# Optimization experiments

Measured on AMD Instinct MI355X. Metric: run time of the kernel, lower is better.

The kernel has to match this reference:

```python
import jax, jax.numpy as jnp
import numpy as np

SCALE_FACTOR = 4.0
DROPOUT_P = 0.5
DROPOUT_KEY = jax.random.key(42)  # fixed key: torch dropout is stochastic; we fix RNG for reproducibility


def setup_inputs() -> dict:
    key = jax.random.key(0)
    k1, k2 = jax.random.split(key)
    x1 = jax.random.normal(k1, (4096, 1024), dtype=jnp.float32)
    x2 = jax.random.normal(k2, (4096, 1024), dtype=jnp.float32)
    return {"x1": x1, "x2": x2}


def reference(x1, x2):
    # scores: [M, N] = x1 @ x2^T, scaled
    scores = jnp.matmul(x1, x2.T) * SCALE_FACTOR
    # F.softmax with no dim on 2-D input -> softmax over dim 1 (keys)
    attn = jax.nn.softmax(scores, axis=-1)
    # dropout p=0.5, train mode (inverted dropout: scale kept units by 1/(1-p))
    keep = jax.random.bernoulli(DROPOUT_KEY, 1.0 - DROPOUT_P, attn.shape)
    attn = jnp.where(keep, attn / (1.0 - DROPOUT_P), 0.0).astype(attn.dtype)
    # output: [M, D] = attn @ x2 (x2 reused as values)
    return jnp.matmul(attn, x2)
```

## Files before the change

### kernel.cpp

```cpp
#include <hip/hip_runtime.h>

typedef unsigned short u16;
typedef unsigned int   u32;
typedef __attribute__((ext_vector_type(4))) float f32x4;
typedef __attribute__((ext_vector_type(8))) short bf16x8;
typedef __attribute__((ext_vector_type(8))) unsigned short u16x8;
typedef __attribute__((ext_vector_type(4))) unsigned short u16x4;

#define MROWS 4096
#define DDIM  1024

__device__ __forceinline__ u16 f2bf(float f) {
  u32 u = __float_as_uint(f);
  return (u16)((u + 0x7FFFu + ((u >> 16) & 1u)) >> 16);
}
__device__ __forceinline__ float bf2f(u16 h) { return __uint_as_float(((u32)h) << 16); }

__device__ __forceinline__ u32 rotl32(u32 x, int r) { return (x << r) | (x >> (32 - r)); }
__device__ __forceinline__ u32 threefry_bits(u32 n) {
  const u32 K0 = 0u, K1 = 42u, K2 = 0x1BD11BDAu ^ 0u ^ 42u;
  u32 x0 = K0;
  u32 x1 = n + K1;
#define TF4(a,b,c,d) \
  x0 += x1; x1 = rotl32(x1, a); x1 ^= x0; \
  x0 += x1; x1 = rotl32(x1, b); x1 ^= x0; \
  x0 += x1; x1 = rotl32(x1, c); x1 ^= x0; \
  x0 += x1; x1 = rotl32(x1, d); x1 ^= x0;
  TF4(13,15,26,6);  x0 += K1; x1 += K2 + 1u;
  TF4(17,29,16,24); x0 += K2; x1 += K0 + 2u;
  TF4(13,15,26,6);  x0 += K0; x1 += K1 + 3u;
  TF4(17,29,16,24); x0 += K1; x1 += K2 + 4u;
  TF4(13,15,26,6);  x0 += K2; x1 += K0 + 5u;
#undef TF4
  return x0 ^ x1;
}

__global__ __launch_bounds__(256)
void expandA(const float4* __restrict__ x, u16* __restrict__ out) {
  int t = blockIdx.x * 256 + threadIdx.x;
  float4 v0 = x[(size_t)t * 2], v1 = x[(size_t)t * 2 + 1];
  float vv[8] = {v0.x*4.f, v0.y*4.f, v0.z*4.f, v0.w*4.f,
                 v1.x*4.f, v1.y*4.f, v1.z*4.f, v1.w*4.f};
  u16 o[24];
#pragma unroll
  for (int j = 0; j < 8; ++j) {
    u16 h = f2bf(vv[j]);
    u16 l = f2bf(vv[j] - bf2f(h));
    o[3*j] = h; o[3*j+1] = h; o[3*j+2] = l;
  }
  u16x8* dst = (u16x8*)(out + (size_t)t * 24);
#pragma unroll
  for (int q = 0; q < 3; ++q) {
    u16x8 wv;
#pragma unroll
    for (int j = 0; j < 8; ++j) wv[j] = o[q*8+j];
    dst[q] = wv;
  }
}

__global__ __launch_bounds__(256)
void castB_transpose(const float* __restrict__ x2, u16* __restrict__ XB,
                     u16* __restrict__ VT) {
  __shared__ float tile[64][65];
  int tid = threadIdx.x;
  int dt = blockIdx.x;
  int kt = blockIdx.y;
#pragma unroll
  for (int it = 0; it < 16; ++it) {
    int lin = it * 256 + tid;
    int r = lin >> 6, c = lin & 63;
    tile[r][c] = x2[(size_t)(kt*64 + r) * DDIM + dt*64 + c];
  }
  __syncthreads();
#pragma unroll
  for (int itr = 0; itr < 2; ++itr) {
    int r  = (tid >> 3) + itr * 32;
    int c0 = (tid & 7) * 8;
    u16 o[24];
#pragma unroll
    for (int j = 0; j < 8; ++j) {
      float v = tile[r][c0 + j];
      u16 h = f2bf(v);
      u16 l = f2bf(v - bf2f(h));
      o[3*j] = h; o[3*j+1] = l; o[3*j+2] = h;
    }
    u16x8* dst = (u16x8*)(XB + (size_t)(kt*64 + r) * 3072 + (size_t)(dt*64 + c0) * 3);
#pragma unroll
    for (int q = 0; q < 3; ++q) {
      u16x8 wv;
#pragma unroll
      for (int j = 0; j < 8; ++j) wv[j] = o[q*8+j];
      dst[q] = wv;
    }
  }
#pragma unroll
  for (int it = 0; it < 2; ++it) {
    int dr  = (tid >> 3) + it * 32;
    int kc0 = (tid & 7) * 8;
    u16x8 wv;
#pragma unroll
    for (int j = 0; j < 8; ++j) wv[j] = f2bf(tile[kc0 + j][dr]);
    *(u16x8*)(VT + (size_t)(dt*64 + dr) * MROWS + kt*64 + kc0) = wv;
  }
}

__device__ __forceinline__ void gload16(const u16* g, u16* l) {
  __builtin_amdgcn_global_load_lds(
      (const __attribute__((address_space(1))) void*)g,
      (__attribute__((address_space(3))) void*)l, 16, 0, 0);
}

#define BARRIER() do { asm volatile("" ::: "memory"); __builtin_amdgcn_s_barrier(); \
                       asm volatile("" ::: "memory"); } while (0)
#define VMCNT(N)  asm volatile("s_waitcnt vmcnt(" #N ")" ::: "memory")
#define PRIO1()   __builtin_amdgcn_s_setprio(1)
#define PRIO0()   __builtin_amdgcn_s_setprio(0)

__device__ __forceinline__ void mma_quad(f32x4 (&acc)[8][4], const bf16x8 (&aF)[4][2],
                                         const bf16x8 (&bF)[2][2], int MH, int NH) {
#pragma unroll
  for (int kx = 0; kx < 2; ++kx)
#pragma unroll
    for (int m = 0; m < 4; ++m)
#pragma unroll
      for (int n = 0; n < 2; ++n)
        acc[MH*4+m][NH*2+n] = __builtin_amdgcn_mfma_f32_16x16x32_bf16(
            aF[m][kx], bF[n][kx], acc[MH*4+m][NH*2+n], 0, 0, 0);
}

template <bool OUT16, bool REMAP>
__device__ __forceinline__ void gemm_body(const u16* __restrict__ A,
                                          const u16* __restrict__ Bt,
                                          void* __restrict__ Cv,
                                          int M, int N, int K, int ntpc) {
  __shared__ u16 smem[65536];
  const int tid = threadIdx.x;
  const int lane = tid & 63;
  const int w = tid >> 6;
  const int wr = w >> 2;
  const int wc = w & 3;
  const int fr = lane & 15;
  const int hi = lane >> 4;

  int bxi, byi;
  if (REMAP) {
    const int id0 = blockIdx.y * gridDim.x + blockIdx.x;
    const int c = id0 & 7, j = id0 >> 3;
    bxi = j >> 1;
    byi = c * 2 + (j & 1);
  } else {
    bxi = blockIdx.x; byi = blockIdx.y;
  }

  const long bm = (long)byi * 256;
  const long bn = (long)bxi * 256;
  const size_t kcol0 = (size_t)blockIdx.z * ntpc * 64;

  const int srow = tid >> 3;
  const int scol = (((tid & 7) ^ (srow & 7)) << 3);
  const u16* Abase = A  + (size_t)(bm + srow) * K + kcol0 + scol;
  const u16* Bbase = Bt + (size_t)(bn + srow) * K + kcol0 + scol;

  const int csw0 = ((hi)     ^ (fr & 7)) << 3;
  const int csw1 = ((4 + hi) ^ (fr & 7)) << 3;
  const int arow = (wr*16 + fr) * 64;
  const int brow = (wc*16 + fr) * 64;

#define RD_A2(dst, D, H, M0) do { \
    const u16* _p = smem + ((D)*2+(H))*8192 + arow + (M0)*2048; \
    dst[M0][0]   = *(const bf16x8*)(_p + csw0); \
    dst[M0][1]   = *(const bf16x8*)(_p + csw1); \
    dst[M0+1][0] = *(const bf16x8*)(_p + 2048 + csw0); \
    dst[M0+1][1] = *(const bf16x8*)(_p + 2048 + csw1); } while (0)
#define RD_B(dst, D, H) do { \
    const u16* _p = smem + 32768 + ((D)*2+(H))*8192 + brow; \
    dst[0][0] = *(const bf16x8*)(_p + csw0); \
    dst[0][1] = *(const bf16x8*)(_p + csw1); \
    dst[1][0] = *(const bf16x8*)(_p + 4096 + csw0); \
    dst[1][1] = *(const bf16x8*)(_p + 4096 + csw1); } while (0)

  f32x4 acc[8][4];
#pragma unroll
  for (int m = 0; m < 8; ++m)
#pragma unroll
    for (int n = 0; n < 4; ++n) acc[m][n] = (f32x4){0.f, 0.f, 0.f, 0.f};
  bf16x8 a0[4][2], a1[4][2], b0[2][2], b1[2][2];

#define STAGE_A(TAU,H,D) do { \
    const u16* _s = Abase + (size_t)(H)*128*K + (size_t)(TAU)*64; \
    u16* _d = smem + ((D)*2+(H))*8192 + tid*8; \
    gload16(_s, _d); gload16(_s + (size_t)64*K, _d + 4096); } while (0)
#define STAGE_B(TAU,H,D) do { \
    const u16* _s = Bbase + (size_t)(H)*128*K + (size_t)(TAU)*64; \
    u16* _d = smem + 32768 + ((D)*2+(H))*8192 + tid*8; \
    gload16(_s, _d); gload16(_s + (size_t)64*K, _d + 4096); } while (0)

  STAGE_A(0,0,0); STAGE_B(0,0,0);
  STAGE_B(0,1,0); STAGE_A(0,1,0);
  VMCNT(0); BARRIER();
  RD_A2(a0,0,0,0); RD_A2(a0,0,0,2); RD_B(b0,0,0);
  STAGE_A(1,0,1); STAGE_B(1,0,1);
  STAGE_B(1,1,1);
  STAGE_A(1,1,1);
  BARRIER();

  const int nt = ntpc;
  for (int T = 0; T < nt; T += 2) {
    const int t2 = (T + 2 < nt) ? T + 2 : nt - 1;
    const int t3 = (T + 3 < nt) ? T + 3 : nt - 1;

    RD_B(b1, 0, 1); RD_A2(a1, 0, 1, 0);
    PRIO1(); mma_quad(acc, a0, b0, 0, 0); PRIO0();
    BARRIER();
    RD_A2(a1, 0, 1, 2);
    STAGE_A(t2, 0, 0); STAGE_B(t2, 0, 0);
    PRIO1(); mma_quad(acc, a0, b1, 0, 1); PRIO0();
    VMCNT(10); BARRIER();
    RD_A2(a0, 1, 0, 0);
    STAGE_B(t2, 1, 0);
    PRIO1(); mma_quad(acc, a1, b0, 1, 0); PRIO0();
    VMCNT(10); BARRIER();
    RD_A2(a0, 1, 0, 2); RD_B(b0, 1, 0);
    STAGE_A(t2, 1, 0);
    PRIO1(); mma_quad(acc, a1, b1, 1, 1); PRIO0();
    VMCNT(8); BARRIER();
    RD_B(b1, 1, 1); RD_A2(a1, 1, 1, 0);
    PRIO1(); mma_quad(acc, a0, b0, 0, 0); PRIO0();
    BARRIER();
    RD_A2(a1, 1, 1, 2);
    STAGE_A(t3, 0, 1); STAGE_B(t3, 0, 1);
    PRIO1(); mma_quad(acc, a0, b1, 0, 1); PRIO0();
    VMCNT(10); BARRIER();
    RD_A2(a0, 0, 0, 0);
    STAGE_B(t3, 1, 1);
    PRIO1(); mma_quad(acc, a1, b0, 1, 0); PRIO0();
    VMCNT(10); BARRIER();
    RD_A2(a0, 0, 0, 2); RD_B(b0, 0, 0);
    STAGE_A(t3, 1, 1);
    PRIO1(); mma_quad(acc, a1, b1, 1, 1); PRIO0();
    VMCNT(8); BARRIER();
  }
#undef STAGE_A
#undef STAGE_B
#undef RD_A2
#undef RD_B

#pragma unroll
  for (int m = 0; m < 8; ++m)
#pragma unroll
    for (int n = 0; n < 4; ++n) {
      size_t row0 = (size_t)(bm + m*32 + wr*16 + hi*4);
      size_t col  = (size_t)(bn + n*64 + wc*16 + fr);
#pragma unroll
      for (int r = 0; r < 4; ++r) {
        if (OUT16) {
          u16* Cz = (u16*)Cv + (size_t)blockIdx.z * (size_t)M * N;
          Cz[(row0 + r) * N + col] = f2bf(acc[m][n][r]);
        } else {
          float* Cz = (float*)Cv + (size_t)blockIdx.z * (size_t)M * N;
          Cz[(row0 + r) * N + col] = acc[m][n][r];
        }
      }
    }
}

__global__ __launch_bounds__(512, 2)
void gemm_qk(const u16* __restrict__ A, const u16* __restrict__ Bt,
             void* __restrict__ Cv, int M, int N, int K, int ntpc) {
  gemm_body<false, false>(A, Bt, Cv, M, N, K, ntpc);
}
__global__ __launch_bounds__(512, 2)
void gemm_pv(const u16* __restrict__ A, const u16* __restrict__ Bt,
             void* __restrict__ Cv, int M, int N, int K, int ntpc) {
  gemm_body<true, true>(A, Bt, Cv, M, N, K, ntpc);
}

__global__ __launch_bounds__(256)
void softmax_dropout(const float* __restrict__ S, u16* __restrict__ P) {
  const int tid  = threadIdx.x;
  const int lane = tid & 63;
  const int w    = tid >> 6;
  const int row  = blockIdx.x * 4 + w;
  const float4* Sr = (const float4*)(S + (size_t)row * MROWS);
  float4 v[16];
#pragma unroll
  for (int i = 0; i < 16; ++i) v[i] = Sr[i * 64 + lane];
  float m = -3.0e38f;
#pragma unroll
  for (int i = 0; i < 16; ++i)
    m = fmaxf(m, fmaxf(fmaxf(v[i].x, v[i].y), fmaxf(v[i].z, v[i].w)));
#pragma unroll
  for (int off = 32; off > 0; off >>= 1) m = fmaxf(m, __shfl_xor(m, off, 64));
  float s = 0.0f;
#pragma unroll
  for (int i = 0; i < 16; ++i) {
    v[i].x = __expf(v[i].x - m); v[i].y = __expf(v[i].y - m);
    v[i].z = __expf(v[i].z - m); v[i].w = __expf(v[i].w - m);
    s += v[i].x + v[i].y + v[i].z + v[i].w;
  }
#pragma unroll
  for (int off = 32; off > 0; off >>= 1) s += __shfl_xor(s, off, 64);
  const float inv = 2.0f / s;
  u16* Pr = P + (size_t)row * MROWS;
#pragma unroll
  for (int i = 0; i < 16; ++i) {
    int j0 = (i * 64 + lane) * 4;
    u32 base = (u32)row * 4096u + (u32)j0;
    float e[4] = {v[i].x, v[i].y, v[i].z, v[i].w};
    u16x4 o;
#pragma unroll
    for (int c = 0; c < 4; ++c) {
      u32 bits = threefry_bits(base + (u32)c);
      float val = (bits & 0x80000000u) ? 0.0f : e[c] * inv;
      o[c] = f2bf(val);
    }
    *(u16x4*)(Pr + j0) = o;
  }
}

__global__ __launch_bounds__(256)
void reduce4(const u16* __restrict__ p, float4* __restrict__ out) {
  size_t i = (size_t)blockIdx.x * 256 + threadIdx.x;
  const size_t NP = (size_t)MROWS * DDIM;
  u16x4 a = *(const u16x4*)(p + i*4);
  u16x4 b = *(const u16x4*)(p + NP + i*4);
  u16x4 c = *(const u16x4*)(p + 2*NP + i*4);
  u16x4 d = *(const u16x4*)(p + 3*NP + i*4);
  float4 r;
  r.x = bf2f(a[0]) + bf2f(b[0]) + bf2f(c[0]) + bf2f(d[0]);
  r.y = bf2f(a[1]) + bf2f(b[1]) + bf2f(c[1]) + bf2f(d[1]);
  r.z = bf2f(a[2]) + bf2f(b[2]) + bf2f(c[2]) + bf2f(d[2]);
  r.w = bf2f(a[3]) + bf2f(b[3]) + bf2f(c[3]) + bf2f(d[3]);
  out[i] = r;
}

extern "C" void kernel_launch(void* const* d_in, const int* in_sizes, int n_in,
                              void* d_out, int out_size, void* d_ws, size_t ws_size,
                              hipStream_t stream) {
  const float* x1 = (const float*)d_in[0];
  const float* x2 = (const float*)d_in[1];
  float* out = (float*)d_out;
  char* ws = (char*)d_ws;

  const size_t OFF_XB   = 25165824;
  const size_t OFF_VT   = 50331648;
  const size_t OFF_S    = 58720256;
  const size_t NEED     = 125829120;
  if (ws_size < NEED) {
    hipMemsetAsync(d_out, 0x7F, (size_t)out_size * sizeof(float), stream);
    return;
  }
  u16*   XA = (u16*)(ws);
  u16*   XB = (u16*)(ws + OFF_XB);
  u16*   VT = (u16*)(ws + OFF_VT);
  float* S  = (float*)(ws + OFF_S);
  u16*   PT = (u16*)(ws + OFF_S);
  u16*   P  = (u16*)(ws);

  expandA<<<2048, 256, 0, stream>>>((const float4*)x1, XA);
  castB_transpose<<<dim3(16, 64), 256, 0, stream>>>(x2, XB, VT);
  gemm_qk<<<dim3(16, 16, 1), 512, 0, stream>>>(XA, XB, S, 4096, 4096, 3072, 48);
  softmax_dropout<<<1024, 256, 0, stream>>>(S, P);
  gemm_pv<<<dim3(4, 16, 4), 512, 0, stream>>>(P, VT, PT, 4096, 1024, 4096, 16);
  reduce4<<<4096, 256, 0, stream>>>(PT, (float4*)out);
}
```

Before: 186.4 us.

## Restructure GEMM to 256x128 tiles, 4 waves, triple-buffered BK=32 pipeline

Replaces the 256x256, 8-wave, double-buffered BK=64 GEMM with a 256x128 tile computed by 4 waves (each 128x64), using a three-stage LDS ring of BK=32 slices and a simpler two-phase loop. Both GEMMs now launch twice as many blocks, and a generalized XCD-aware block remap replaces the old one. The aim is a smaller LDS footprint, more blocks for occupancy, and a simpler prefetch schedule. In exchange each block reuses fewer bytes per tile and runs more K iterations.

```diff
diff --git a/kernel.cpp b/kernel.cpp
--- a/kernel.cpp
+++ b/kernel.cpp
@@ -116,141 +116,107 @@
 #define PRIO1()   __builtin_amdgcn_s_setprio(1)
 #define PRIO0()   __builtin_amdgcn_s_setprio(0)
 
-__device__ __forceinline__ void mma_quad(f32x4 (&acc)[8][4], const bf16x8 (&aF)[4][2],
-                                         const bf16x8 (&bF)[2][2], int MH, int NH) {
-#pragma unroll
-  for (int kx = 0; kx < 2; ++kx)
-#pragma unroll
-    for (int m = 0; m < 4; ++m)
-#pragma unroll
-      for (int n = 0; n < 2; ++n)
-        acc[MH*4+m][NH*2+n] = __builtin_amdgcn_mfma_f32_16x16x32_bf16(
-            aF[m][kx], bF[n][kx], acc[MH*4+m][NH*2+n], 0, 0, 0);
-}
-
-template <bool OUT16, bool REMAP>
+template <bool OUT16>
 __device__ __forceinline__ void gemm_body(const u16* __restrict__ A,
                                           const u16* __restrict__ Bt,
                                           void* __restrict__ Cv,
-                                          int M, int N, int K, int ntpc) {
-  __shared__ u16 smem[65536];
-  const int tid = threadIdx.x;
+                                          int M, int N, int K, int ntpc, int gxlog) {
+  __shared__ u16 smem[36864];
+  const int tid  = threadIdx.x;
   const int lane = tid & 63;
-  const int w = tid >> 6;
-  const int wr = w >> 2;
-  const int wc = w & 3;
+  const int w    = tid >> 6;
+  const int wm = w >> 1;
+  const int wn = w & 1;
   const int fr = lane & 15;
   const int hi = lane >> 4;
 
-  int bxi, byi;
-  if (REMAP) {
-    const int id0 = blockIdx.y * gridDim.x + blockIdx.x;
-    const int c = id0 & 7, j = id0 >> 3;
-    bxi = j >> 1;
-    byi = c * 2 + (j & 1);
-  } else {
-    bxi = blockIdx.x; byi = blockIdx.y;
-  }
+  const int id0 = blockIdx.y * gridDim.x + blockIdx.x;
+  const int xcd = id0 & 7, j = id0 >> 3;
+  const int bxi = j & (gridDim.x - 1);
+  const int byi = xcd * (gridDim.y >> 3) + (j >> gxlog);
 
   const long bm = (long)byi * 256;
-  const long bn = (long)bxi * 256;
-  const size_t kcol0 = (size_t)blockIdx.z * ntpc * 64;
-
-  const int srow = tid >> 3;
-  const int scol = (((tid & 7) ^ (srow & 7)) << 3);
-  const u16* Abase = A  + (size_t)(bm + srow) * K + kcol0 + scol;
-  const u16* Bbase = Bt + (size_t)(bn + srow) * K + kcol0 + scol;
-
-  const int csw0 = ((hi)     ^ (fr & 7)) << 3;
-  const int csw1 = ((4 + hi) ^ (fr & 7)) << 3;
-  const int arow = (wr*16 + fr) * 64;
-  const int brow = (wc*16 + fr) * 64;
-
-#define RD_A2(dst, D, H, M0) do { \
-    const u16* _p = smem + ((D)*2+(H))*8192 + arow + (M0)*2048; \
-    dst[M0][0]   = *(const bf16x8*)(_p + csw0); \
-    dst[M0][1]   = *(const bf16x8*)(_p + csw1); \
-    dst[M0+1][0] = *(const bf16x8*)(_p + 2048 + csw0); \
-    dst[M0+1][1] = *(const bf16x8*)(_p + 2048 + csw1); } while (0)
-#define RD_B(dst, D, H) do { \
-    const u16* _p = smem + 32768 + ((D)*2+(H))*8192 + brow; \
-    dst[0][0] = *(const bf16x8*)(_p + csw0); \
-    dst[0][1] = *(const bf16x8*)(_p + csw1); \
-    dst[1][0] = *(const bf16x8*)(_p + 4096 + csw0); \
-    dst[1][1] = *(const bf16x8*)(_p + 4096 + csw1); } while (0)
+  const long bn = (long)bxi * 128;
+  const size_t kcol0 = (size_t)blockIdx.z * ntpc * 32;
+
+  const int srow = lane >> 2;
+  const int schunk = (lane & 3) ^ (srow & 3);
+  const u16* asrc = A  + (size_t)(bm + w*64 + srow) * K + kcol0 + schunk*8;
+  const u16* bsrc = Bt + (size_t)(bn + w*32 + srow) * K + kcol0 + schunk*8;
+
+  const int csw  = (hi ^ (fr & 3)) << 3;
+  const int aoff = (wm*128 + fr) * 32 + csw;
+  const int boff = 8192 + (wn*64 + fr) * 32 + csw;
+  const int adst = w*2048 + lane*8;
+  const int bdst = 8192 + w*1024 + lane*8;
 
   f32x4 acc[8][4];
 #pragma unroll
   for (int m = 0; m < 8; ++m)
 #pragma unroll
     for (int n = 0; n < 4; ++n) acc[m][n] = (f32x4){0.f, 0.f, 0.f, 0.f};
-  bf16x8 a0[4][2], a1[4][2], b0[2][2], b1[2][2];
-
-#define STAGE_A(TAU,H,D) do { \
-    const u16* _s = Abase + (size_t)(H)*128*K + (size_t)(TAU)*64; \
-    u16* _d = smem + ((D)*2+(H))*8192 + tid*8; \
-    gload16(_s, _d); gload16(_s + (size_t)64*K, _d + 4096); } while (0)
-#define STAGE_B(TAU,H,D) do { \
-    const u16* _s = Bbase + (size_t)(H)*128*K + (size_t)(TAU)*64; \
-    u16* _d = smem + 32768 + ((D)*2+(H))*8192 + tid*8; \
-    gload16(_s, _d); gload16(_s + (size_t)64*K, _d + 4096); } while (0)
-
-  STAGE_A(0,0,0); STAGE_B(0,0,0);
-  STAGE_B(0,1,0); STAGE_A(0,1,0);
-  VMCNT(0); BARRIER();
-  RD_A2(a0,0,0,0); RD_A2(a0,0,0,2); RD_B(b0,0,0);
-  STAGE_A(1,0,1); STAGE_B(1,0,1);
-  STAGE_B(1,1,1);
-  STAGE_A(1,1,1);
-  BARRIER();
+  bf16x8 a0[8], a1[8], b0[4], b1[4];
+
+#define STAGE(TAU, LB) do { \
+    const u16* _a = asrc + (size_t)(TAU)*32; \
+    const u16* _b = bsrc + (size_t)(TAU)*32; \
+    gload16(_a,                 smem + (LB) + adst); \
+    gload16(_a + (size_t)16*K,  smem + (LB) + adst + 512); \
+    gload16(_a + (size_t)32*K,  smem + (LB) + adst + 1024); \
+    gload16(_a + (size_t)48*K,  smem + (LB) + adst + 1536); \
+    gload16(_b,                 smem + (LB) + bdst); \
+    gload16(_b + (size_t)16*K,  smem + (LB) + bdst + 512); } while (0)
+
+#define RD(dA, dB, LB) do { \
+    const u16* _pa = smem + (LB) + aoff; \
+    const u16* _pb = smem + (LB) + boff; \
+    dA[0] = *(const bf16x8*)(_pa);        dA[1] = *(const bf16x8*)(_pa + 512); \
+    dA[2] = *(const bf16x8*)(_pa + 1024); dA[3] = *(const bf16x8*)(_pa + 1536); \
+    dA[4] = *(const bf16x8*)(_pa + 2048); dA[5] = *(const bf16x8*)(_pa + 2560); \
+    dA[6] = *(const bf16x8*)(_pa + 3072); dA[7] = *(const bf16x8*)(_pa + 3584); \
+    dB[0] = *(const bf16x8*)(_pb);        dB[1] = *(const bf16x8*)(_pb + 512); \
+    dB[2] = *(const bf16x8*)(_pb + 1024); dB[3] = *(const bf16x8*)(_pb + 1536); } while (0)
+
+#define MMA(aa, bb) do { PRIO1(); \
+    _Pragma("unroll") \
+    for (int m = 0; m < 8; ++m) \
+      _Pragma("unroll") \
+      for (int n = 0; n < 4; ++n) \
+        acc[m][n] = __builtin_amdgcn_mfma_f32_16x16x32_bf16(aa[m], bb[n], acc[m][n], 0, 0, 0); \
+    PRIO0(); } while (0)
+
+  u32 lb0 = 0, lb1 = 12288, lb2 = 24576;
+
+  STAGE(0, lb0); STAGE(1, lb1); STAGE(2, lb2);
+  VMCNT(12); BARRIER();
+  RD(a0, b0, lb0);
+  VMCNT(6); BARRIER();
 
   const int nt = ntpc;
   for (int T = 0; T < nt; T += 2) {
-    const int t2 = (T + 2 < nt) ? T + 2 : nt - 1;
     const int t3 = (T + 3 < nt) ? T + 3 : nt - 1;
-
-    RD_B(b1, 0, 1); RD_A2(a1, 0, 1, 0);
-    PRIO1(); mma_quad(acc, a0, b0, 0, 0); PRIO0();
-    BARRIER();
-    RD_A2(a1, 0, 1, 2);
-    STAGE_A(t2, 0, 0); STAGE_B(t2, 0, 0);
-    PRIO1(); mma_quad(acc, a0, b1, 0, 1); PRIO0();
-    VMCNT(10); BARRIER();
-    RD_A2(a0, 1, 0, 0);
-    STAGE_B(t2, 1, 0);
-    PRIO1(); mma_quad(acc, a1, b0, 1, 0); PRIO0();
-    VMCNT(10); BARRIER();
-    RD_A2(a0, 1, 0, 2); RD_B(b0, 1, 0);
-    STAGE_A(t2, 1, 0);
-    PRIO1(); mma_quad(acc, a1, b1, 1, 1); PRIO0();
-    VMCNT(8); BARRIER();
-    RD_B(b1, 1, 1); RD_A2(a1, 1, 1, 0);
-    PRIO1(); mma_quad(acc, a0, b0, 0, 0); PRIO0();
-    BARRIER();
-    RD_A2(a1, 1, 1, 2);
-    STAGE_A(t3, 0, 1); STAGE_B(t3, 0, 1);
-    PRIO1(); mma_quad(acc, a0, b1, 0, 1); PRIO0();
-    VMCNT(10); BARRIER();
-    RD_A2(a0, 0, 0, 0);
-    STAGE_B(t3, 1, 1);
-    PRIO1(); mma_quad(acc, a1, b0, 1, 0); PRIO0();
-    VMCNT(10); BARRIER();
-    RD_A2(a0, 0, 0, 2); RD_B(b0, 0, 0);
-    STAGE_A(t3, 1, 1);
-    PRIO1(); mma_quad(acc, a1, b1, 1, 1); PRIO0();
-    VMCNT(8); BARRIER();
-  }
-#undef STAGE_A
-#undef STAGE_B
-#undef RD_A2
-#undef RD_B
+    const int t4 = (T + 4 < nt) ? T + 4 : nt - 1;
+
+    RD(a1, b1, lb1);
+    STAGE(t3, lb0);
+    MMA(a0, b0);
+    VMCNT(6); BARRIER();
+    RD(a0, b0, lb2);
+    STAGE(t4, lb1);
+    MMA(a1, b1);
+    VMCNT(6); BARRIER();
+    u32 tmp = lb2; lb2 = lb1; lb1 = lb0; lb0 = tmp;
+  }
+#undef STAGE
+#undef RD
+#undef MMA
 
 #pragma unroll
   for (int m = 0; m < 8; ++m)
 #pragma unroll
     for (int n = 0; n < 4; ++n) {
-      size_t row0 = (size_t)(bm + m*32 + wr*16 + hi*4);
-      size_t col  = (size_t)(bn + n*64 + wc*16 + fr);
+      size_t row0 = (size_t)(bm + wm*128 + m*16 + hi*4);
+      size_t col  = (size_t)(bn + wn*64 + n*16 + fr);
 #pragma unroll
       for (int r = 0; r < 4; ++r) {
         if (OUT16) {
@@ -264,15 +230,15 @@
     }
 }
 
-__global__ __launch_bounds__(512, 2)
+__global__ __launch_bounds__(256, 2)
 void gemm_qk(const u16* __restrict__ A, const u16* __restrict__ Bt,
              void* __restrict__ Cv, int M, int N, int K, int ntpc) {
-  gemm_body<false, false>(A, Bt, Cv, M, N, K, ntpc);
-}
-__global__ __launch_bounds__(512, 2)
+  gemm_body<false>(A, Bt, Cv, M, N, K, ntpc, 5);
+}
+__global__ __launch_bounds__(256, 2)
 void gemm_pv(const u16* __restrict__ A, const u16* __restrict__ Bt,
              void* __restrict__ Cv, int M, int N, int K, int ntpc) {
-  gemm_body<true, true>(A, Bt, Cv, M, N, K, ntpc);
+  gemm_body<true>(A, Bt, Cv, M, N, K, ntpc, 3);
 }
 
 __global__ __launch_bounds__(256)
@@ -359,8 +325,8 @@
 
   expandA<<<2048, 256, 0, stream>>>((const float4*)x1, XA);
   castB_transpose<<<dim3(16, 64), 256, 0, stream>>>(x2, XB, VT);
-  gemm_qk<<<dim3(16, 16, 1), 512, 0, stream>>>(XA, XB, S, 4096, 4096, 3072, 48);
+  gemm_qk<<<dim3(32, 16, 1), 256, 0, stream>>>(XA, XB, S, 4096, 4096, 3072, 96);
   softmax_dropout<<<1024, 256, 0, stream>>>(S, P);
-  gemm_pv<<<dim3(4, 16, 4), 512, 0, stream>>>(P, VT, PT, 4096, 1024, 4096, 16);
+  gemm_pv<<<dim3(8, 16, 4), 256, 0, stream>>>(P, VT, PT, 4096, 1024, 4096, 32);
   reduce4<<<4096, 256, 0, stream>>>(PT, (float4*)out);
 }
```

Measured after the change: 220.7 us. 1.18x slower.
